# Kernel optimization log

Hardware: AMD Instinct MI355X
Metric: run time of the kernel (lower is better)

The kernel has to match this reference:

```python
import jax, jax.numpy as jnp
import numpy as np

H, W = 2000, 1000  # T_out buffer: (1, 2000, 1000); conv spatial grid matches
FILL = -9999.0


def _winit(k, o, c):
    return jax.random.normal(k, (o, c), jnp.float32) * (1.0 / np.sqrt(c))


def setup_inputs() -> dict:
    key = jax.random.key(0)
    ks = jax.random.split(key, 6)
    inp = jax.random.normal(ks[0], (1, 9, H, W), dtype=jnp.float32)
    T_out = jnp.zeros((1, H, W), dtype=jnp.float32)
    flat = jnp.arange(H * W, dtype=jnp.int32)
    T_indices = jnp.stack([flat // W, flat % W]).reshape(2, H, W)
    return {
        "input": inp,
        "T_out": T_out,
        "T_indices": T_indices,
        "w1": _winit(ks[1], 18, 9), "b1": jnp.zeros((18,), jnp.float32),
        "w2": _winit(ks[2], 36, 18), "b2": jnp.zeros((36,), jnp.float32),
        "w3": _winit(ks[3], 36, 36), "b3": jnp.zeros((36,), jnp.float32),
        "w4": _winit(ks[4], 1, 36), "b4": jnp.zeros((1,), jnp.float32),
    }


def _conv1x1(x, w, b):
    # 1x1 conv == channel matmul: x (b,c,h,w), w (o,c)
    return jnp.einsum('bchw,oc->bohw', x, w) + b[None, :, None, None]


def reference(input, T_out, T_indices, w1, b1, w2, b2, w3, b3, w4, b4):
    x = jax.nn.relu(_conv1x1(input, w1, b1))
    x = jax.nn.relu(_conv1x1(x, w2, b2))
    x = jax.nn.relu(_conv1x1(x, w3, b3))
    x = _conv1x1(x, w4, b4)  # (1,1,H,W)
    # fill buffer with -9999 then indexed scatter of the fused scores
    T = jnp.full(T_out.shape, FILL, dtype=T_out.dtype)
    T = T.at[:, T_indices[0], T_indices[1]].set(x[0, 0])
    # MaxPool2d([1,1000]) -> max over W; MaxPool2d([2000,1]) -> max over H
    out1 = T.max(axis=2).squeeze()  # (2000,)
    out2 = T.max(axis=1).squeeze()  # (1000,)
    return (out1, out2)
```

## Files before the change

kernel.cpp:

```cpp
#include <hip/hip_runtime.h>

typedef _Float16 f16x8 __attribute__((ext_vector_type(8)));
typedef _Float16 f16x4 __attribute__((ext_vector_type(4)));
typedef __fp16 h16x2 __attribute__((ext_vector_type(2)));
typedef float f32x4 __attribute__((ext_vector_type(4)));

#define HH 2000
#define WW 1000
#define HWSZ (HH * WW)
#define NEG_INF (-3.0e38f)

__device__ __forceinline__ unsigned fenc(float f) {
    unsigned u = __float_as_uint(f);
    return (u & 0x80000000u) ? ~u : (u | 0x80000000u);
}
__device__ __forceinline__ float fdec(unsigned k) {
    unsigned u = (k & 0x80000000u) ? (k & 0x7fffffffu) : ~k;
    return __uint_as_float(u);
}

__global__ void decode_buckets(unsigned* __restrict__ buck, int n) {
    int i = blockIdx.x * blockDim.x + threadIdx.x;
    if (i < n) {
        unsigned k = buck[i];
        ((float*)buck)[i] = fdec(k);
    }
}


__global__ __launch_bounds__(128) void mlp_max_mfma(
    const float* __restrict__ in,
    const float* __restrict__ w1, const float* __restrict__ b1,
    const float* __restrict__ w2, const float* __restrict__ b2,
    const float* __restrict__ w3, const float* __restrict__ b3,
    const float* __restrict__ w4, const float* __restrict__ b4,
    unsigned* __restrict__ rowbuck, unsigned* __restrict__ colbuck) {
    __shared__ _Float16 lds[2][2 * 1280];
    __shared__ float rowsm[2][16][16];

    const int tx = threadIdx.x;
    const int wv = threadIdx.y;
    const int px = tx & 15;
    const int q = tx >> 4;

    _Float16* s0buf1 = &lds[wv][0];
    _Float16* s0buf2 = &lds[wv][640];
    _Float16* s1buf1 = &lds[wv][1280];
    _Float16* s1buf2 = &lds[wv][1920];

    f16x8 A1[2], A2[3], A3s0[3], A3s1[3];
#pragma unroll
    for (int t = 0; t < 2; ++t) {
        const int m = t * 16 + px;
#pragma unroll
        for (int j = 0; j < 8; ++j) {
            const int k = q * 8 + j;
            float v = 0.f;
            if (m < 18) {
                if (k < 9) v = w1[m * 9 + k];
                else if (k == 9) v = b1[m];
            }
            A1[t][j] = (_Float16)v;
        }
    }
#pragma unroll
    for (int t = 0; t < 3; ++t) {
        const int m = t * 16 + px;
#pragma unroll
        for (int j = 0; j < 8; ++j) {
            const int k = q * 8 + j;
            float v = 0.f;
            if (m < 36) {
                if (k < 18) v = w2[m * 18 + k];
                else if (k == 18) v = b2[m];
            }
            A2[t][j] = (_Float16)v;
        }
    }
#pragma unroll
    for (int t = 0; t < 3; ++t) {
        const int m = t * 16 + px;
#pragma unroll
        for (int j = 0; j < 8; ++j) {
            const int k = q * 8 + j;
            float v = 0.f;
            if (m < 36 && k < 32) v = w3[m * 36 + k];
            A3s0[t][j] = (_Float16)v;
            float v2 = 0.f;
            const int k2 = 32 + k;
            if (m < 36) {
                if (k2 < 36) v2 = w3[m * 36 + k2];
                else if (k2 == 36) v2 = b3[m];
            }
            A3s1[t][j] = (_Float16)v2;
        }
    }

    float w4r[3][4];
#pragma unroll
    for (int t = 0; t < 3; ++t)
#pragma unroll
        for (int rg = 0; rg < 4; ++rg) {
            const int ch = t * 16 + q * 4 + rg;
            w4r[t][rg] = (ch < 36) ? w4[ch] : 0.f;
        }
    const float b4s = b4[0];

    const int col = blockIdx.x * 32 + wv * 16 + px;
    const int colc = (col < WW) ? col : (WW - 1);
    const bool colok = (col < WW);
    const int rb = blockIdx.y * 16;

    float colmax = NEG_INF;
    const f32x4 zf4 = {0.f, 0.f, 0.f, 0.f};
    const h16x2 z2 = {(__fp16)0.f, (__fp16)0.f};

    const float* pin = in + colc;

    union U8 { f16x8 v; h16x2 h[4]; };
    union U4 { f16x4 v; h16x2 h[2]; };

    float ca[8], cb[8], na[8], nb[8];

    auto LOAD = [&](int r, float (&v0)[8], float (&v1)[8]) {
#pragma unroll
        for (int j = 0; j < 8; ++j) {
            const int c = q * 8 + j;
            float x0 = 0.f, x1 = 0.f;
            if (c < 9) {
                x0 = pin[c * HWSZ + r * WW];
                x1 = pin[c * HWSZ + r * WW + WW];
            } else if (c == 9) {
                x0 = 1.f; x1 = 1.f;
            }
            v0[j] = x0;
            v1[j] = x1;
        }
    };

    auto COMPUTE = [&](int it, const float (&v0)[8], const float (&v1)[8]) {
        U8 b0u, b1u;
#pragma unroll
        for (int j = 0; j < 4; ++j) {
            b0u.h[j] = __builtin_amdgcn_cvt_pkrtz(v0[2 * j], v0[2 * j + 1]);
            b1u.h[j] = __builtin_amdgcn_cvt_pkrtz(v1[2 * j], v1[2 * j + 1]);
        }
        const f16x8 bin0 = b0u.v;
        const f16x8 bin1 = b1u.v;

        f32x4 D1a[2], D1b[2];
#pragma unroll
        for (int t = 0; t < 2; ++t) {
            D1a[t] = __builtin_amdgcn_mfma_f32_16x16x32_f16(A1[t], bin0, zf4, 0, 0, 0);
            D1b[t] = __builtin_amdgcn_mfma_f32_16x16x32_f16(A1[t], bin1, zf4, 0, 0, 0);
        }
#pragma unroll
        for (int t = 0; t < 2; ++t) {
            U4 h0, h1;
            h0.h[0] = __builtin_elementwise_max(
                __builtin_amdgcn_cvt_pkrtz(D1a[t][0], D1a[t][1]), z2);
            h0.h[1] = __builtin_elementwise_max(
                __builtin_amdgcn_cvt_pkrtz(D1a[t][2], D1a[t][3]), z2);
            h1.h[0] = __builtin_elementwise_max(
                __builtin_amdgcn_cvt_pkrtz(D1b[t][0], D1b[t][1]), z2);
            h1.h[1] = __builtin_elementwise_max(
                __builtin_amdgcn_cvt_pkrtz(D1b[t][2], D1b[t][3]), z2);
            if (t == 1 && q == 0) {
                h0.v[2] = (_Float16)1.f;
                h1.v[2] = (_Float16)1.f;
            }
            *(f16x4*)&s0buf1[px * 40 + t * 16 + q * 4] = h0.v;
            *(f16x4*)&s1buf1[px * 40 + t * 16 + q * 4] = h1.v;
        }
        const f16x8 B2a = *(const f16x8*)&s0buf1[px * 40 + q * 8];
        const f16x8 B2b = *(const f16x8*)&s1buf1[px * 40 + q * 8];

        f32x4 D2a[3], D2b[3];
#pragma unroll
        for (int t = 0; t < 3; ++t) {
            D2a[t] = __builtin_amdgcn_mfma_f32_16x16x32_f16(A2[t], B2a, zf4, 0, 0, 0);
            D2b[t] = __builtin_amdgcn_mfma_f32_16x16x32_f16(A2[t], B2b, zf4, 0, 0, 0);
        }
#pragma unroll
        for (int t = 0; t < 3; ++t) {
            U4 h0, h1;
            h0.h[0] = __builtin_elementwise_max(
                __builtin_amdgcn_cvt_pkrtz(D2a[t][0], D2a[t][1]), z2);
            h0.h[1] = __builtin_elementwise_max(
                __builtin_amdgcn_cvt_pkrtz(D2a[t][2], D2a[t][3]), z2);
            h1.h[0] = __builtin_elementwise_max(
                __builtin_amdgcn_cvt_pkrtz(D2b[t][0], D2b[t][1]), z2);
            h1.h[1] = __builtin_elementwise_max(
                __builtin_amdgcn_cvt_pkrtz(D2b[t][2], D2b[t][3]), z2);
            if (t < 2) {
                *(f16x4*)&s0buf2[px * 40 + t * 16 + q * 4] = h0.v;
                *(f16x4*)&s1buf2[px * 40 + t * 16 + q * 4] = h1.v;
            } else if (q == 0) {
                *(f16x4*)&s0buf2[px * 40 + 32] = h0.v;
                *(f16x4*)&s1buf2[px * 40 + 32] = h1.v;
            }
        }
        const f16x8 B3a0 = *(const f16x8*)&s0buf2[px * 40 + q * 8];
        const f16x8 B3b0 = *(const f16x8*)&s1buf2[px * 40 + q * 8];
        f16x8 B3a1 = {0, 0, 0, 0, 0, 0, 0, 0};
        f16x8 B3b1 = {0, 0, 0, 0, 0, 0, 0, 0};
        if (q == 0) {
            const f16x4 t0 = *(const f16x4*)&s0buf2[px * 40 + 32];
            const f16x4 t1 = *(const f16x4*)&s1buf2[px * 40 + 32];
#pragma unroll
            for (int j = 0; j < 4; ++j) { B3a1[j] = t0[j]; B3b1[j] = t1[j]; }
            B3a1[4] = (_Float16)1.f;
            B3b1[4] = (_Float16)1.f;
        }

        f32x4 D3a[3], D3b[3];
#pragma unroll
        for (int t = 0; t < 3; ++t) {
            D3a[t] = __builtin_amdgcn_mfma_f32_16x16x32_f16(A3s0[t], B3a0, zf4, 0, 0, 0);
            D3a[t] = __builtin_amdgcn_mfma_f32_16x16x32_f16(A3s1[t], B3a1, D3a[t], 0, 0, 0);
            D3b[t] = __builtin_amdgcn_mfma_f32_16x16x32_f16(A3s0[t], B3b0, zf4, 0, 0, 0);
            D3b[t] = __builtin_amdgcn_mfma_f32_16x16x32_f16(A3s1[t], B3b1, D3b[t], 0, 0, 0);
        }

        float sa = 0.f, sb = 0.f;
#pragma unroll
        for (int t = 0; t < 3; ++t)
#pragma unroll
            for (int rg = 0; rg < 4; ++rg) {
                sa = fmaf(w4r[t][rg], fmaxf(D3a[t][rg], 0.f), sa);
                sb = fmaf(w4r[t][rg], fmaxf(D3b[t][rg], 0.f), sb);
            }
        sa += __shfl_xor(sa, 16, 64); sb += __shfl_xor(sb, 16, 64);
        sa += __shfl_xor(sa, 32, 64); sb += __shfl_xor(sb, 32, 64);
        sa += b4s; sb += b4s;

        sa = colok ? sa : NEG_INF;
        sb = colok ? sb : NEG_INF;
        colmax = fmaxf(colmax, fmaxf(sa, sb));

        if (q == 0) rowsm[wv][it * 2][px] = sa;
        else if (q == 1) rowsm[wv][it * 2 + 1][px] = sb;
    };

    LOAD(rb, ca, cb);
#pragma unroll 1
    for (int it = 0; it < 8; it += 2) {
        LOAD(rb + (it + 1) * 2, na, nb);
        COMPUTE(it, ca, cb);
        if (it < 6) LOAD(rb + (it + 2) * 2, ca, cb);
        COMPUTE(it + 1, na, nb);
    }

    if (q == 0 && colok) atomicMax(&colbuck[col], fenc(colmax));
    if (tx < 16) {
        const f32x4 v0 = *(const f32x4*)&rowsm[wv][tx][0];
        const f32x4 v1 = *(const f32x4*)&rowsm[wv][tx][4];
        const f32x4 v2 = *(const f32x4*)&rowsm[wv][tx][8];
        const f32x4 v3 = *(const f32x4*)&rowsm[wv][tx][12];
        float m = NEG_INF;
#pragma unroll
        for (int j = 0; j < 4; ++j) {
            m = fmaxf(m, fmaxf(fmaxf(v0[j], v1[j]), fmaxf(v2[j], v3[j])));
        }
        atomicMax(&rowbuck[rb + tx], fenc(m));
    }
}

extern "C" void kernel_launch(void* const* d_in, const int* in_sizes, int n_in,
                              void* d_out, int out_size, void* d_ws, size_t ws_size,
                              hipStream_t stream) {
    const float* in = (const float*)d_in[0];
    const float* w1 = (const float*)d_in[3];
    const float* b1 = (const float*)d_in[4];
    const float* w2 = (const float*)d_in[5];
    const float* b2 = (const float*)d_in[6];
    const float* w3 = (const float*)d_in[7];
    const float* b3 = (const float*)d_in[8];
    const float* w4 = (const float*)d_in[9];
    const float* b4 = (const float*)d_in[10];

    unsigned* buck = (unsigned*)d_out;

    (void)hipMemsetAsync(buck, 0, 3000 * sizeof(unsigned), stream);

    dim3 block(64, 2);
    dim3 grid(32, 125);
    mlp_max_mfma<<<grid, block, 0, stream>>>(in, w1, b1, w2, b2, w3, b3, w4, b4,
                                             buck, buck + 2000);

    decode_buckets<<<(3000 + 255) / 256, 256, 0, stream>>>(buck, 3000);
}
```

Before: 188.8 us.

## Stage input tile into LDS via async global_load_lds with staged waitcnt

Replaces per-thread scalar global loads of the 9 input channels with 16-byte global_load_lds transfers. At kernel start each wave issues these for its whole 16-row by 16-column tile into LDS, and the loop then waits on progressively smaller vmcnt values so compute on early rows overlaps the remaining transfers. Lanes that feed the bias and padding channels read from a small constant LDS buffer. This aims to cut the number of memory instructions and hide load latency, at the cost of more LDS use, which may lower occupancy, and of relying on exact vmcnt ordering.

```diff
diff --git a/kernel.cpp b/kernel.cpp
--- a/kernel.cpp
+++ b/kernel.cpp
@@ -25,6 +25,16 @@
         unsigned k = buck[i];
         ((float*)buck)[i] = fdec(k);
     }
+}
+
+template <int N> __device__ __forceinline__ void waitcnt_vm() {
+    asm volatile("s_waitcnt vmcnt(%0)" ::"n"(N) : "memory");
+}
+
+__device__ __forceinline__ void stage16(const float* g, float* l) {
+    __builtin_amdgcn_global_load_lds(
+        (const __attribute__((address_space(1))) void*)g,
+        (__attribute__((address_space(3))) void*)l, 16, 0, 0);
 }
 
 
@@ -35,18 +45,42 @@
     const float* __restrict__ w3, const float* __restrict__ b3,
     const float* __restrict__ w4, const float* __restrict__ b4,
     unsigned* __restrict__ rowbuck, unsigned* __restrict__ colbuck) {
-    __shared__ _Float16 lds[2][2 * 1280];
+    __shared__ float stage[2][2304];
+    __shared__ _Float16 albuf[2][2 * 1280];
     __shared__ float rowsm[2][16][16];
+    __shared__ float zbuf[128];
 
     const int tx = threadIdx.x;
     const int wv = threadIdx.y;
     const int px = tx & 15;
     const int q = tx >> 4;
-
-    _Float16* s0buf1 = &lds[wv][0];
-    _Float16* s0buf2 = &lds[wv][640];
-    _Float16* s1buf1 = &lds[wv][1280];
-    _Float16* s1buf2 = &lds[wv][1920];
+    const int rb = blockIdx.y * 16;
+    const int col0 = blockIdx.x * 32 + wv * 16;
+
+#pragma unroll
+    for (int s = 0; s < 9; ++s) {
+        const int m = s * 64 + tx;
+        const int r = m / 36;
+        const int rem = m - r * 36;
+        const int c = rem >> 2;
+        const int k = rem & 3;
+        int cs = col0 + k * 4;
+        if (cs > WW - 4) cs = WW - 4;
+        stage16(in + (size_t)c * HWSZ + (size_t)(rb + r) * WW + cs,
+                &stage[wv][s * 256]);
+    }
+
+    {
+        float2 zv;
+        zv.x = (tx == 8) ? 1.f : 0.f;
+        zv.y = 0.f;
+        *(float2*)&zbuf[tx * 2] = zv;
+    }
+
+    _Float16* s0buf1 = &albuf[wv][0];
+    _Float16* s0buf2 = &albuf[wv][640];
+    _Float16* s1buf1 = &albuf[wv][1280];
+    _Float16* s1buf2 = &albuf[wv][1920];
 
     f16x8 A1[2], A2[3], A3s0[3], A3s1[3];
 #pragma unroll
@@ -106,44 +140,51 @@
         }
     const float b4s = b4[0];
 
-    const int col = blockIdx.x * 32 + wv * 16 + px;
-    const int colc = (col < WW) ? col : (WW - 1);
+    const int col = col0 + px;
     const bool colok = (col < WW);
-    const int rb = blockIdx.y * 16;
 
     float colmax = NEG_INF;
     const f32x4 zf4 = {0.f, 0.f, 0.f, 0.f};
     const h16x2 z2 = {(__fp16)0.f, (__fp16)0.f};
 
-    const float* pin = in + colc;
-
     union U8 { f16x8 v; h16x2 h[4]; };
     union U4 { f16x4 v; h16x2 h[2]; };
 
-    float ca[8], cb[8], na[8], nb[8];
-
-    auto LOAD = [&](int r, float (&v0)[8], float (&v1)[8]) {
-#pragma unroll
-        for (int j = 0; j < 8; ++j) {
-            const int c = q * 8 + j;
-            float x0 = 0.f, x1 = 0.f;
-            if (c < 9) {
-                x0 = pin[c * HWSZ + r * WW];
-                x1 = pin[c * HWSZ + r * WW + WW];
-            } else if (c == 9) {
-                x0 = 1.f; x1 = 1.f;
-            }
-            v0[j] = x0;
-            v1[j] = x1;
-        }
-    };
-
-    auto COMPUTE = [&](int it, const float (&v0)[8], const float (&v1)[8]) {
+    const float* sw = &stage[wv][0];
+    const int strj = (q == 0) ? 144 : 0;
+    const int str0 = (q <= 1) ? 144 : 0;
+    const float* pj = (q == 0) ? (sw + px) : zbuf;
+    const float* p0 = (q == 0) ? (sw + px) : ((q == 1) ? (sw + 128 + px) : zbuf);
+
+#pragma unroll 1
+    for (int it = 0; it < 8; ++it) {
+        switch (it) {
+            case 0: waitcnt_vm<7>(); break;
+            case 1: waitcnt_vm<6>(); break;
+            case 2: waitcnt_vm<5>(); break;
+            case 3: waitcnt_vm<4>(); break;
+            case 4: waitcnt_vm<3>(); break;
+            case 5: waitcnt_vm<2>(); break;
+            case 6: waitcnt_vm<1>(); break;
+            default: waitcnt_vm<0>(); break;
+        }
+
+        float fa[8], fb[8];
+        fa[0] = p0[0];
+        fb[0] = p0[str0];
+#pragma unroll
+        for (int j = 1; j < 8; ++j) {
+            fa[j] = pj[j * 16];
+            fb[j] = pj[strj + j * 16];
+        }
+        p0 += 2 * str0;
+        pj += 2 * strj;
+
         U8 b0u, b1u;
 #pragma unroll
         for (int j = 0; j < 4; ++j) {
-            b0u.h[j] = __builtin_amdgcn_cvt_pkrtz(v0[2 * j], v0[2 * j + 1]);
-            b1u.h[j] = __builtin_amdgcn_cvt_pkrtz(v1[2 * j], v1[2 * j + 1]);
+            b0u.h[j] = __builtin_amdgcn_cvt_pkrtz(fa[2 * j], fa[2 * j + 1]);
+            b1u.h[j] = __builtin_amdgcn_cvt_pkrtz(fb[2 * j], fb[2 * j + 1]);
         }
         const f16x8 bin0 = b0u.v;
         const f16x8 bin1 = b1u.v;
@@ -240,15 +281,6 @@
 
         if (q == 0) rowsm[wv][it * 2][px] = sa;
         else if (q == 1) rowsm[wv][it * 2 + 1][px] = sb;
-    };
-
-    LOAD(rb, ca, cb);
-#pragma unroll 1
-    for (int it = 0; it < 8; it += 2) {
-        LOAD(rb + (it + 1) * 2, na, nb);
-        COMPUTE(it, ca, cb);
-        if (it < 6) LOAD(rb + (it + 2) * 2, ca, cb);
-        COMPUTE(it + 1, na, nb);
     }
 
     if (q == 0 && colok) atomicMax(&colbuck[col], fenc(colmax));
```

Result: slower. 201.3 us (+6.6%).

## Spread input channels across lanes, preload bias ones, use fdot2 final layer

Applied to the files above, without the earlier changes.

Reorders the layer-1 K dimension so each lane quad loads only 2-3 input channels instead of q==0/1 lanes loading up to 8. This spreads global loads evenly across lanes and cuts per-lane load count and registers. The constant-one bias column for layer 3 is written once into LDS, so the second B fragment becomes a plain 16-byte LDS read. The final 36->1 projection now packs ReLU outputs to fp16 and uses fdot2. That trims VALU work but adds fp16 rounding to the last layer.

```diff
diff --git a/kernel.cpp b/kernel.cpp
--- a/kernel.cpp
+++ b/kernel.cpp
@@ -35,7 +35,7 @@
     const float* __restrict__ w3, const float* __restrict__ b3,
     const float* __restrict__ w4, const float* __restrict__ b4,
     unsigned* __restrict__ rowbuck, unsigned* __restrict__ colbuck) {
-    __shared__ _Float16 lds[2][2 * 1280];
+    __shared__ _Float16 albuf[2][2 * 1280];
     __shared__ float rowsm[2][16][16];
 
     const int tx = threadIdx.x;
@@ -43,10 +43,16 @@
     const int px = tx & 15;
     const int q = tx >> 4;
 
-    _Float16* s0buf1 = &lds[wv][0];
-    _Float16* s0buf2 = &lds[wv][640];
-    _Float16* s1buf1 = &lds[wv][1280];
-    _Float16* s1buf2 = &lds[wv][1920];
+    _Float16* s0buf1 = &albuf[wv][0];
+    _Float16* s0buf2 = &albuf[wv][640];
+    _Float16* s1buf1 = &albuf[wv][1280];
+    _Float16* s1buf2 = &albuf[wv][1920];
+
+    if (q == 0) {
+        const f16x4 binit = {(_Float16)1.f, (_Float16)0.f, (_Float16)0.f, (_Float16)0.f};
+        *(f16x4*)&s0buf2[px * 40 + 36] = binit;
+        *(f16x4*)&s1buf2[px * 40 + 36] = binit;
+    }
 
     f16x8 A1[2], A2[3], A3s0[3], A3s1[3];
 #pragma unroll
@@ -54,11 +60,14 @@
         const int m = t * 16 + px;
 #pragma unroll
         for (int j = 0; j < 8; ++j) {
-            const int k = q * 8 + j;
             float v = 0.f;
             if (m < 18) {
-                if (k < 9) v = w1[m * 9 + k];
-                else if (k == 9) v = b1[m];
+                if (j == 0) v = w1[m * 9 + q];
+                else if (j == 1) v = w1[m * 9 + 4 + q];
+                else if (j == 2) {
+                    if (q == 0) v = w1[m * 9 + 8];
+                    else if (q == 1) v = b1[m];
+                }
             }
             A1[t][j] = (_Float16)v;
         }
@@ -96,13 +105,15 @@
         }
     }
 
-    float w4r[3][4];
+    h16x2 w4p[3][2];
 #pragma unroll
     for (int t = 0; t < 3; ++t)
 #pragma unroll
-        for (int rg = 0; rg < 4; ++rg) {
-            const int ch = t * 16 + q * 4 + rg;
-            w4r[t][rg] = (ch < 36) ? w4[ch] : 0.f;
+        for (int i = 0; i < 2; ++i) {
+            const int c0 = t * 16 + q * 4 + 2 * i;
+            const int c1 = c0 + 1;
+            w4p[t][i] = __builtin_amdgcn_cvt_pkrtz(c0 < 36 ? w4[c0] : 0.f,
+                                                   c1 < 36 ? w4[c1] : 0.f);
         }
     const float b4s = b4[0];
 
@@ -115,36 +126,33 @@
     const f32x4 zf4 = {0.f, 0.f, 0.f, 0.f};
     const h16x2 z2 = {(__fp16)0.f, (__fp16)0.f};
 
-    const float* pin = in + colc;
-
     union U8 { f16x8 v; h16x2 h[4]; };
     union U4 { f16x4 v; h16x2 h[2]; };
 
-    float ca[8], cb[8], na[8], nb[8];
-
-    auto LOAD = [&](int r, float (&v0)[8], float (&v1)[8]) {
-#pragma unroll
-        for (int j = 0; j < 8; ++j) {
-            const int c = q * 8 + j;
-            float x0 = 0.f, x1 = 0.f;
-            if (c < 9) {
-                x0 = pin[c * HWSZ + r * WW];
-                x1 = pin[c * HWSZ + r * WW + WW];
-            } else if (c == 9) {
-                x0 = 1.f; x1 = 1.f;
-            }
-            v0[j] = x0;
-            v1[j] = x1;
-        }
+    const int off0 = q * HWSZ + colc;
+    const int off1 = (4 + q) * HWSZ + colc;
+    const int off2 = 8 * HWSZ + colc;
+    const float j2fill = (q == 1) ? 1.f : 0.f;
+
+    float ca[3], cb[3], na[3], nb[3];
+
+    auto LOAD = [&](int r, float (&v0)[3], float (&v1)[3]) {
+        const float* rbase = in + (size_t)r * WW;
+        v0[0] = rbase[off0]; v1[0] = rbase[off0 + WW];
+        v0[1] = rbase[off1]; v1[1] = rbase[off1 + WW];
+        float x0 = j2fill, x1 = j2fill;
+        if (q == 0) { x0 = rbase[off2]; x1 = rbase[off2 + WW]; }
+        v0[2] = x0; v1[2] = x1;
     };
 
-    auto COMPUTE = [&](int it, const float (&v0)[8], const float (&v1)[8]) {
+    auto COMPUTE = [&](int it, const float (&v0)[3], const float (&v1)[3]) {
         U8 b0u, b1u;
-#pragma unroll
-        for (int j = 0; j < 4; ++j) {
-            b0u.h[j] = __builtin_amdgcn_cvt_pkrtz(v0[2 * j], v0[2 * j + 1]);
-            b1u.h[j] = __builtin_amdgcn_cvt_pkrtz(v1[2 * j], v1[2 * j + 1]);
-        }
+        b0u.h[0] = __builtin_amdgcn_cvt_pkrtz(v0[0], v0[1]);
+        b0u.h[1] = __builtin_amdgcn_cvt_pkrtz(v0[2], 0.f);
+        b0u.h[2] = z2; b0u.h[3] = z2;
+        b1u.h[0] = __builtin_amdgcn_cvt_pkrtz(v1[0], v1[1]);
+        b1u.h[1] = __builtin_amdgcn_cvt_pkrtz(v1[2], 0.f);
+        b1u.h[2] = z2; b1u.h[3] = z2;
         const f16x8 bin0 = b0u.v;
         const f16x8 bin1 = b1u.v;
 
@@ -202,16 +210,8 @@
         }
         const f16x8 B3a0 = *(const f16x8*)&s0buf2[px * 40 + q * 8];
         const f16x8 B3b0 = *(const f16x8*)&s1buf2[px * 40 + q * 8];
-        f16x8 B3a1 = {0, 0, 0, 0, 0, 0, 0, 0};
-        f16x8 B3b1 = {0, 0, 0, 0, 0, 0, 0, 0};
-        if (q == 0) {
-            const f16x4 t0 = *(const f16x4*)&s0buf2[px * 40 + 32];
-            const f16x4 t1 = *(const f16x4*)&s1buf2[px * 40 + 32];
-#pragma unroll
-            for (int j = 0; j < 4; ++j) { B3a1[j] = t0[j]; B3b1[j] = t1[j]; }
-            B3a1[4] = (_Float16)1.f;
-            B3b1[4] = (_Float16)1.f;
-        }
+        const f16x8 B3a1 = *(const f16x8*)&s0buf2[px * 40 + 32];
+        const f16x8 B3b1 = *(const f16x8*)&s1buf2[px * 40 + 32];
 
         f32x4 D3a[3], D3b[3];
 #pragma unroll
@@ -222,14 +222,24 @@
             D3b[t] = __builtin_amdgcn_mfma_f32_16x16x32_f16(A3s1[t], B3b1, D3b[t], 0, 0, 0);
         }
 
-        float sa = 0.f, sb = 0.f;
-#pragma unroll
-        for (int t = 0; t < 3; ++t)
-#pragma unroll
-            for (int rg = 0; rg < 4; ++rg) {
-                sa = fmaf(w4r[t][rg], fmaxf(D3a[t][rg], 0.f), sa);
-                sb = fmaf(w4r[t][rg], fmaxf(D3b[t][rg], 0.f), sb);
-            }
+        float sa0 = 0.f, sa1 = 0.f, sb0 = 0.f, sb1 = 0.f;
+#pragma unroll
+        for (int t = 0; t < 3; ++t) {
+            const h16x2 pa0 = __builtin_elementwise_max(
+                __builtin_amdgcn_cvt_pkrtz(D3a[t][0], D3a[t][1]), z2);
+            const h16x2 pa1 = __builtin_elementwise_max(
+                __builtin_amdgcn_cvt_pkrtz(D3a[t][2], D3a[t][3]), z2);
+            const h16x2 pb0 = __builtin_elementwise_max(
+                __builtin_amdgcn_cvt_pkrtz(D3b[t][0], D3b[t][1]), z2);
+            const h16x2 pb1 = __builtin_elementwise_max(
+                __builtin_amdgcn_cvt_pkrtz(D3b[t][2], D3b[t][3]), z2);
+            sa0 = __builtin_amdgcn_fdot2(pa0, w4p[t][0], sa0, false);
+            sa1 = __builtin_amdgcn_fdot2(pa1, w4p[t][1], sa1, false);
+            sb0 = __builtin_amdgcn_fdot2(pb0, w4p[t][0], sb0, false);
+            sb1 = __builtin_amdgcn_fdot2(pb1, w4p[t][1], sb1, false);
+        }
+        float sa = sa0 + sa1;
+        float sb = sb0 + sb1;
         sa += __shfl_xor(sa, 16, 64); sb += __shfl_xor(sb, 16, 64);
         sa += __shfl_xor(sa, 32, 64); sb += __shfl_xor(sb, 32, 64);
         sa += b4s; sb += b4s;
```

New measurement: 182.5 us. -3.3%, faster.
